# Optimization experiments

Measured on AMD Instinct MI355X. Metric: run time of the kernel, lower is better.

The kernel has to match this reference:

```python
import jax, jax.numpy as jnp
import numpy as np
import math

B, S, D, H = 4, 2048, 768, 12
HD = D // H  # 64


def setup_inputs() -> dict:
    key = jax.random.key(0)
    ks = jax.random.split(key, 9)
    s = 0.02
    return {
        "hidden_states": jax.random.normal(ks[0], (B, S, D), jnp.float32),
        "layout_q": jax.random.normal(ks[1], (B, S, D), jnp.float32),
        "layout_k": jax.random.normal(ks[2], (B, S, D), jnp.float32),
        "attention_mask": jnp.zeros((B, 1, 1, S), jnp.float32),
        "Wq": jax.random.normal(ks[3], (D, D), jnp.float32) * s,
        "bq": jnp.zeros((D,), jnp.float32),
        "Wk": jax.random.normal(ks[4], (D, D), jnp.float32) * s,
        "bk": jnp.zeros((D,), jnp.float32),
        "Wv": jax.random.normal(ks[5], (D, D), jnp.float32) * s,
        "bv": jnp.zeros((D,), jnp.float32),
    }


def _split_heads(x):
    # [B,S,D] -> [B,H,S,HD]
    return x.reshape(B, S, H, HD).transpose(0, 2, 1, 3)


def reference(hidden_states, layout_q, layout_k, attention_mask, Wq, bq, Wk, bk, Wv, bv):
    q = _split_heads(hidden_states @ Wq.T + bq)
    k = _split_heads(hidden_states @ Wk.T + bk)
    v = _split_heads(hidden_states @ Wv.T + bv)
    lq = _split_heads(layout_q)
    lk = _split_heads(layout_k)
    scale = 1.0 / math.sqrt(HD)
    # dual-stream scores: content + layout, both [B,H,S,S]
    scores = (jnp.einsum("bhqd,bhkd->bhqk", q, k)
              + jnp.einsum("bhqd,bhkd->bhqk", lq, lk)) * scale
    scores = scores + attention_mask
    probs = jax.nn.softmax(scores, axis=-1)
    ctx = jnp.einsum("bhqk,bhkd->bhqd", probs, v)
    return ctx.transpose(0, 2, 1, 3).reshape(B, S, D)
```

## Files before the change

kernel.cpp:

```cpp
#include <hip/hip_runtime.h>


typedef __attribute__((ext_vector_type(8))) short short8;
typedef __attribute__((ext_vector_type(4))) short short4v;
typedef __attribute__((ext_vector_type(4))) float floatx4;

#define LOG2E 1.4426950408889634f
#define QSCL 0.18033688011112042f

static constexpr int Sn = 2048, Dn = 768, Hn = 12, BHn = 48;

__device__ __forceinline__ unsigned short f2bf(float f) {
  unsigned u = __float_as_uint(f);
  u += 0x7FFFu + ((u >> 16) & 1u);
  return (unsigned short)(u >> 16);
}

typedef const __attribute__((address_space(1))) unsigned int* gas_t;
typedef __attribute__((address_space(3))) unsigned int* las_t;
__device__ __forceinline__ void async16(const void* g, void* l) {
  __builtin_amdgcn_global_load_lds((gas_t)g, (las_t)l, 16, 0, 0);
}

__device__ __forceinline__ floatx4 mfma16(short4v a, short4v b, floatx4 c) {
#if __has_builtin(__builtin_amdgcn_mfma_f32_16x16x16bf16_1k)
  return __builtin_amdgcn_mfma_f32_16x16x16bf16_1k(a, b, c, 0, 0, 0);
#else
  asm volatile("v_mfma_f32_16x16x16_bf16 %0, %1, %2, %0" : "+v"(c) : "v"(a), "v"(b));
  return c;
#endif
}

__global__ void cast_hs_kernel(const float* __restrict__ in, unsigned short* __restrict__ out, int n4) {
  int i = blockIdx.x * 256 + threadIdx.x;
  if (i >= n4) return;
  float4 v = ((const float4*)in)[i];
  ushort4 o = make_ushort4(f2bf(v.x), f2bf(v.y), f2bf(v.z), f2bf(v.w));
  ((ushort4*)out)[i] = o;
}

__global__ void cast_w_kernel(const float* __restrict__ w0, const float* __restrict__ w1,
                              const float* __restrict__ w2, unsigned short* __restrict__ out) {
  int i = blockIdx.x * 256 + threadIdx.x;
  const float* src = (blockIdx.y == 0) ? w0 : (blockIdx.y == 1) ? w1 : w2;
  float4 v = ((const float4*)src)[i];
  ushort4 o = make_ushort4(f2bf(v.x), f2bf(v.y), f2bf(v.z), f2bf(v.w));
  ((ushort4*)(out + (size_t)blockIdx.y * Dn * Dn))[i] = o;
}

__global__ void pack_layout_kernel(const float* __restrict__ lq, const float* __restrict__ lk,
                                   unsigned short* __restrict__ Qc, unsigned short* __restrict__ Kc) {
  int idx = blockIdx.x * 256 + threadIdx.x;
  const float* src = blockIdx.y ? lk : lq;
  unsigned short* dst = blockIdx.y ? Kc : Qc;
  const float sc = blockIdx.y ? 1.0f : QSCL;
  int d4 = idx & 15;
  int t = idx >> 4;
  int h = t % Hn;
  int bs = t / Hn;
  int b = bs >> 11, s = bs & (Sn - 1);
  float4 v = ((const float4*)src)[idx];
  ushort4 o = make_ushort4(f2bf(v.x * sc), f2bf(v.y * sc), f2bf(v.z * sc), f2bf(v.w * sc));
  size_t off = ((size_t)(b * Hn + h) * Sn + s) * 128 + 64 + d4 * 4;
  *(ushort4*)(dst + off) = o;
}

__global__ __launch_bounds__(256, 2)
void proj_kernel(const unsigned short* __restrict__ X,
                 const unsigned short* __restrict__ Wb,
                 const float* __restrict__ bq, const float* __restrict__ bk, const float* __restrict__ bv,
                 unsigned short* __restrict__ Qc, unsigned short* __restrict__ Kc,
                 unsigned short* __restrict__ Vt) {
  __shared__ __align__(16) unsigned short sMem[16384];
  unsigned short* const sA = sMem;
  unsigned short* const sB = sMem + 8192;

  const int z = blockIdx.z;
  const unsigned short* W = Wb + (size_t)z * Dn * Dn;
  const float* bias = (z == 0) ? bq : (z == 1) ? bk : bv;

  const int t = threadIdx.x;
  const int lane = t & 63, wave = t >> 6;
  const int wm = wave >> 1, wn = wave & 1;
  const int quad = lane >> 4, col15 = lane & 15;
  const int m0 = blockIdx.y * 128, n0 = blockIdx.x * 128;

  const int srow = lane >> 3, schunk = lane & 7;

  floatx4 acc[4][4];
#pragma unroll
  for (int i = 0; i < 4; i++)
#pragma unroll
    for (int j = 0; j < 4; j++) acc[i][j] = (floatx4){0.f, 0.f, 0.f, 0.f};

  for (int k0 = 0; k0 < Dn; k0 += 64) {
    __syncthreads();
#pragma unroll
    for (int c = 0; c < 4; c++) {
      int row = wave * 32 + c * 8 + srow;
      int g = schunk ^ (row & 7);
      async16(X + (size_t)(m0 + row) * Dn + k0 + g * 8, sA + (wave * 32 + c * 8) * 64);
      async16(W + (size_t)(n0 + row) * Dn + k0 + g * 8, sB + (wave * 32 + c * 8) * 64);
    }
    __syncthreads();
#pragma unroll
    for (int kk = 0; kk < 2; kk++) {
      short8 af[4], bf[4];
      const int slot_ = ((kk * 4 + quad) ^ (col15 & 7)) * 8;
#pragma unroll
      for (int i = 0; i < 4; i++)
        af[i] = *(const short8*)(sA + (wm * 64 + i * 16 + col15) * 64 + slot_);
#pragma unroll
      for (int j = 0; j < 4; j++)
        bf[j] = *(const short8*)(sB + (wn * 64 + j * 16 + col15) * 64 + slot_);
#pragma unroll
      for (int i = 0; i < 4; i++)
#pragma unroll
        for (int j = 0; j < 4; j++)
          acc[i][j] = __builtin_amdgcn_mfma_f32_16x16x32_bf16(af[i], bf[j], acc[i][j], 0, 0, 0);
    }
  }

  __syncthreads();
  const int b = m0 >> 11;
  const int s0g = m0 & (Sn - 1);
  const int h0 = n0 >> 6;

  if (z < 2) {
    const float scl = (z == 0) ? QSCL : 1.0f;
    unsigned short* dst0 = (z == 0) ? Qc : Kc;
#pragma unroll
    for (int j = 0; j < 4; j++) {
      int nl = wn * 64 + j * 16 + col15;
      float bias_n = bias[n0 + nl];
#pragma unroll
      for (int i = 0; i < 4; i++) {
        int mb = wm * 64 + i * 16 + quad * 4;
#pragma unroll
        for (int r = 0; r < 4; r++) {
          int m = mb + r;
          sMem[m * 128 + (nl ^ (((m >> 2) & 3) << 4))] = f2bf((acc[i][j][r] + bias_n) * scl);
        }
      }
    }
    __syncthreads();
#pragma unroll
    for (int cc = 0; cc < 8; cc++) {
      int idx = cc * 256 + t;
      int m = idx >> 4, piece = idx & 15;
      int h = h0 + (piece >> 3), d8 = piece & 7;
      short8 v = *(const short8*)(sMem + m * 128 + (piece ^ (((m >> 2) & 3) << 1)) * 8);
      *(short8*)(dst0 + ((size_t)(b * Hn + h) * Sn + s0g + m) * 128 + d8 * 8) = v;
    }
  } else {
#pragma unroll
    for (int j = 0; j < 4; j++) {
      int nl = wn * 64 + j * 16 + col15;
      float bias_n = bias[n0 + nl];
#pragma unroll
      for (int i = 0; i < 4; i++) {
        int mb = wm * 64 + i * 16 + quad * 4;
        ushort4 pk = make_ushort4(f2bf(acc[i][j][0] + bias_n), f2bf(acc[i][j][1] + bias_n),
                                  f2bf(acc[i][j][2] + bias_n), f2bf(acc[i][j][3] + bias_n));
        *(ushort4*)(sMem + nl * 128 + (mb ^ ((nl & 7) << 4))) = pk;
      }
    }
    __syncthreads();
#pragma unroll
    for (int cc = 0; cc < 8; cc++) {
      int idx = cc * 256 + t;
      int nl = idx >> 4, piece = idx & 15;
      int h = h0 + (nl >> 6), d = nl & 63;
      short8 v = *(const short8*)(sMem + nl * 128 + (piece ^ ((nl & 7) << 1)) * 8);
      *(short8*)(Vt + ((size_t)(b * Hn + h) * 64 + d) * Sn + s0g + piece * 8) = v;
    }
  }
}

__global__ __launch_bounds__(256, 3)
void attn_kernel(const unsigned short* __restrict__ Qc,
                 const unsigned short* __restrict__ Kc,
                 const unsigned short* __restrict__ Vt,
                 const float* __restrict__ mask,
                 float* __restrict__ out) {
  __shared__ __align__(16) unsigned short sKc[64 * 128];
  __shared__ __align__(16) unsigned short sVt[64 * 64];
  __shared__ __align__(16) float sMask[Sn];

  const int t = threadIdx.x;
  const int lane = t & 63, wave = t >> 6;
  const int quad = lane >> 4, col15 = lane & 15;

  const int id = blockIdx.x;
  const int slot = id >> 3;
  const int bh = (id & 7) + 8 * (slot >> 4);
  const int q0 = (slot & 15) * 128;
  const int b = bh / Hn, h = bh % Hn;

  const float* mbase = mask + (size_t)b * Sn;
#pragma unroll
  for (int c = 0; c < 2; c++)
    async16(mbase + (c * 256 + wave * 64 + lane) * 4, sMask + (c * 256 + wave * 64) * 4);

  short8 aq[2][4];
  const unsigned short* Qbase = Qc + ((size_t)bh * Sn + q0 + wave * 32) * 128;
#pragma unroll
  for (int jq = 0; jq < 2; jq++)
#pragma unroll
    for (int kk = 0; kk < 4; kk++)
      aq[jq][kk] = *(const short8*)(Qbase + (size_t)(jq * 16 + col15) * 128 + kk * 32 + quad * 8);

  floatx4 OT[4][2];
#pragma unroll
  for (int i = 0; i < 4; i++) {
    OT[i][0] = (floatx4){0.f, 0.f, 0.f, 0.f};
    OT[i][1] = (floatx4){0.f, 0.f, 0.f, 0.f};
  }
  float lsum[2] = {0.f, 0.f};

  const unsigned short* Kbase = Kc + (size_t)bh * Sn * 128;
  const unsigned short* Vbase = Vt + (size_t)bh * 64 * Sn;

  const int krow = lane >> 4, kslot = lane & 15;
  const int vrow = lane >> 3, vslot = lane & 7;

  for (int kt = 0; kt < Sn / 64; kt++) {
    __syncthreads();
#pragma unroll
    for (int c = 0; c < 4; c++) {
      int row = wave * 16 + c * 4 + krow;
      int g = (kslot & 8) | ((kslot ^ row) & 7);
      async16(Kbase + (size_t)(kt * 64 + row) * 128 + g * 8, sKc + (wave * 16 + c * 4) * 128);
    }
#pragma unroll
    for (int c = 0; c < 2; c++) {
      int row = wave * 16 + c * 8 + vrow;
      int g = vslot ^ (row & 7);
      async16(Vbase + (size_t)row * Sn + kt * 64 + g * 8, sVt + (wave * 16 + c * 8) * 64);
    }
    __syncthreads();

    floatx4 sacc[4][2];
#pragma unroll
    for (int jk = 0; jk < 4; jk++) {
      sacc[jk][0] = (floatx4){0.f, 0.f, 0.f, 0.f};
      sacc[jk][1] = (floatx4){0.f, 0.f, 0.f, 0.f};
#pragma unroll
      for (int kk = 0; kk < 4; kk++) {
        int gr = kk * 4 + quad;
        int slot_ = ((gr & 8) | ((gr ^ col15) & 7)) * 8;
        short8 kf = *(const short8*)(sKc + (jk * 16 + col15) * 128 + slot_);
        sacc[jk][0] = __builtin_amdgcn_mfma_f32_16x16x32_bf16(kf, aq[0][kk], sacc[jk][0], 0, 0, 0);
        sacc[jk][1] = __builtin_amdgcn_mfma_f32_16x16x32_bf16(kf, aq[1][kk], sacc[jk][1], 0, 0, 0);
      }
    }

    short4v pvb[2][4];
#pragma unroll
    for (int jk = 0; jk < 4; jk++) {
      float4 mv = *(const float4*)(sMask + kt * 64 + jk * 16 + quad * 4);
      float m0 = mv.x * LOG2E, m1 = mv.y * LOG2E, m2 = mv.z * LOG2E, m3 = mv.w * LOG2E;
#pragma unroll
      for (int jq = 0; jq < 2; jq++) {
        unsigned u0 = __float_as_uint(__builtin_amdgcn_exp2f(sacc[jk][jq][0] + m0)) & 0xFFFF0000u;
        unsigned u1 = __float_as_uint(__builtin_amdgcn_exp2f(sacc[jk][jq][1] + m1)) & 0xFFFF0000u;
        unsigned u2 = __float_as_uint(__builtin_amdgcn_exp2f(sacc[jk][jq][2] + m2)) & 0xFFFF0000u;
        unsigned u3 = __float_as_uint(__builtin_amdgcn_exp2f(sacc[jk][jq][3] + m3)) & 0xFFFF0000u;
        lsum[jq] += (__uint_as_float(u0) + __uint_as_float(u1)) +
                    (__uint_as_float(u2) + __uint_as_float(u3));
        int2 pk;
        pk.x = (int)((u0 >> 16) | u1);
        pk.y = (int)((u2 >> 16) | u3);
        pvb[jq][jk] = *(short4v*)&pk;
      }
    }

#pragma unroll
    for (int i = 0; i < 4; i++) {
      int row = i * 16 + col15;
#pragma unroll
      for (int jk = 0; jk < 4; jk++) {
        int gi = (jk * 2 + (quad >> 1)) ^ (row & 7);
        short4v vf = *(const short4v*)(sVt + row * 64 + gi * 8 + (quad & 1) * 4);
        OT[i][0] = mfma16(vf, pvb[0][jk], OT[i][0]);
        OT[i][1] = mfma16(vf, pvb[1][jk], OT[i][1]);
      }
    }
  }

  float linv[2];
#pragma unroll
  for (int jq = 0; jq < 2; jq++) {
    float s_ = lsum[jq];
    s_ += __shfl_xor(s_, 16);
    s_ += __shfl_xor(s_, 32);
    linv[jq] = 1.0f / s_;
  }
#pragma unroll
  for (int jq = 0; jq < 2; jq++) {
    float* obase = out + ((size_t)b * Sn + q0 + wave * 32 + jq * 16 + col15) * Dn + h * 64 + quad * 4;
#pragma unroll
    for (int i = 0; i < 4; i++) {
      float4 o;
      o.x = OT[i][jq][0] * linv[jq];
      o.y = OT[i][jq][1] * linv[jq];
      o.z = OT[i][jq][2] * linv[jq];
      o.w = OT[i][jq][3] * linv[jq];
      *(float4*)(obase + i * 16) = o;
    }
  }
}

extern "C" void kernel_launch(void* const* d_in, const int* in_sizes, int n_in,
                              void* d_out, int out_size, void* d_ws, size_t ws_size,
                              hipStream_t stream) {
  const float* hs   = (const float*)d_in[0];
  const float* lq   = (const float*)d_in[1];
  const float* lk   = (const float*)d_in[2];
  const float* mask = (const float*)d_in[3];
  const float* Wq   = (const float*)d_in[4];
  const float* bq   = (const float*)d_in[5];
  const float* Wk   = (const float*)d_in[6];
  const float* bk   = (const float*)d_in[7];
  const float* Wv   = (const float*)d_in[8];
  const float* bv   = (const float*)d_in[9];
  float* out = (float*)d_out;

  char* ws = (char*)d_ws;
  unsigned short* Xbf = (unsigned short*)ws;
  unsigned short* Wbf = (unsigned short*)(ws + 12582912);
  unsigned short* Qc  = (unsigned short*)(ws + 12582912 + 3538944);
  unsigned short* Kc  = Qc + (size_t)BHn * Sn * 128;
  unsigned short* Vt  = Kc + (size_t)BHn * Sn * 128;

  cast_hs_kernel<<<6144, 256, 0, stream>>>(hs, Xbf, 1572864);
  cast_w_kernel<<<dim3(576, 3), 256, 0, stream>>>(Wq, Wk, Wv, Wbf);
  pack_layout_kernel<<<dim3(6144, 2), 256, 0, stream>>>(lq, lk, Qc, Kc);
  proj_kernel<<<dim3(6, 64, 3), 256, 0, stream>>>(Xbf, Wbf, bq, bk, bv, Qc, Kc, Vt);
  attn_kernel<<<768, 256, 0, stream>>>(Qc, Kc, Vt, mask, out);
}
```

Baseline: 272.9 us.

## Fuse fp32 casts and layout packing into projection; use 16x16x32 MFMA for PV

Drops the three standalone cast and pack kernels. The projection GEMM now loads fp32 X and W directly, converts them to bf16 in registers before storing to LDS, and packs the scaled layout_q/layout_k halves into Qc/Kc in its epilogue. In attention, probabilities are staged through a padded LDS buffer so the PV product can use the wider 16x16x32 bf16 MFMA instead of 16x16x16. This removes kernel launches and intermediate bf16 round trips through memory. In exchange, the GEMM loses its async global-to-LDS loads in favour of synchronous register loads with no prefetch, and attention uses more LDS per block, which may reduce occupancy.

After: 281.8 us. 3.3% more time.

```diff
diff --git a/kernel.cpp b/kernel.cpp
--- a/kernel.cpp
+++ b/kernel.cpp
@@ -1,8 +1,8 @@
 #include <hip/hip_runtime.h>
+#include <hip/hip_bf16.h>
 
 
 typedef __attribute__((ext_vector_type(8))) short short8;
-typedef __attribute__((ext_vector_type(4))) short short4v;
 typedef __attribute__((ext_vector_type(4))) float floatx4;
 
 #define LOG2E 1.4426950408889634f
@@ -16,59 +16,31 @@
   return (unsigned short)(u >> 16);
 }
 
+__device__ __forceinline__ short8 cvt8(float4 a, float4 b) {
+  union { __hip_bfloat162 h; int i; } u0, u1, u2, u3;
+  u0.h = __float22bfloat162_rn(float2{a.x, a.y});
+  u1.h = __float22bfloat162_rn(float2{a.z, a.w});
+  u2.h = __float22bfloat162_rn(float2{b.x, b.y});
+  u3.h = __float22bfloat162_rn(float2{b.z, b.w});
+  short8 r;
+  ((int*)&r)[0] = u0.i; ((int*)&r)[1] = u1.i;
+  ((int*)&r)[2] = u2.i; ((int*)&r)[3] = u3.i;
+  return r;
+}
+
 typedef const __attribute__((address_space(1))) unsigned int* gas_t;
 typedef __attribute__((address_space(3))) unsigned int* las_t;
 __device__ __forceinline__ void async16(const void* g, void* l) {
   __builtin_amdgcn_global_load_lds((gas_t)g, (las_t)l, 16, 0, 0);
 }
 
-__device__ __forceinline__ floatx4 mfma16(short4v a, short4v b, floatx4 c) {
-#if __has_builtin(__builtin_amdgcn_mfma_f32_16x16x16bf16_1k)
-  return __builtin_amdgcn_mfma_f32_16x16x16bf16_1k(a, b, c, 0, 0, 0);
-#else
-  asm volatile("v_mfma_f32_16x16x16_bf16 %0, %1, %2, %0" : "+v"(c) : "v"(a), "v"(b));
-  return c;
-#endif
-}
-
-__global__ void cast_hs_kernel(const float* __restrict__ in, unsigned short* __restrict__ out, int n4) {
-  int i = blockIdx.x * 256 + threadIdx.x;
-  if (i >= n4) return;
-  float4 v = ((const float4*)in)[i];
-  ushort4 o = make_ushort4(f2bf(v.x), f2bf(v.y), f2bf(v.z), f2bf(v.w));
-  ((ushort4*)out)[i] = o;
-}
-
-__global__ void cast_w_kernel(const float* __restrict__ w0, const float* __restrict__ w1,
-                              const float* __restrict__ w2, unsigned short* __restrict__ out) {
-  int i = blockIdx.x * 256 + threadIdx.x;
-  const float* src = (blockIdx.y == 0) ? w0 : (blockIdx.y == 1) ? w1 : w2;
-  float4 v = ((const float4*)src)[i];
-  ushort4 o = make_ushort4(f2bf(v.x), f2bf(v.y), f2bf(v.z), f2bf(v.w));
-  ((ushort4*)(out + (size_t)blockIdx.y * Dn * Dn))[i] = o;
-}
-
-__global__ void pack_layout_kernel(const float* __restrict__ lq, const float* __restrict__ lk,
-                                   unsigned short* __restrict__ Qc, unsigned short* __restrict__ Kc) {
-  int idx = blockIdx.x * 256 + threadIdx.x;
-  const float* src = blockIdx.y ? lk : lq;
-  unsigned short* dst = blockIdx.y ? Kc : Qc;
-  const float sc = blockIdx.y ? 1.0f : QSCL;
-  int d4 = idx & 15;
-  int t = idx >> 4;
-  int h = t % Hn;
-  int bs = t / Hn;
-  int b = bs >> 11, s = bs & (Sn - 1);
-  float4 v = ((const float4*)src)[idx];
-  ushort4 o = make_ushort4(f2bf(v.x * sc), f2bf(v.y * sc), f2bf(v.z * sc), f2bf(v.w * sc));
-  size_t off = ((size_t)(b * Hn + h) * Sn + s) * 128 + 64 + d4 * 4;
-  *(ushort4*)(dst + off) = o;
-}
-
 __global__ __launch_bounds__(256, 2)
-void proj_kernel(const unsigned short* __restrict__ X,
-                 const unsigned short* __restrict__ Wb,
-                 const float* __restrict__ bq, const float* __restrict__ bk, const float* __restrict__ bv,
+void proj_kernel(const float* __restrict__ X,
+                 const float* __restrict__ Wq, const float* __restrict__ Wk,
+                 const float* __restrict__ Wv,
+                 const float* __restrict__ bq, const float* __restrict__ bk,
+                 const float* __restrict__ bv,
+                 const float* __restrict__ LQ, const float* __restrict__ LK,
                  unsigned short* __restrict__ Qc, unsigned short* __restrict__ Kc,
                  unsigned short* __restrict__ Vt) {
   __shared__ __align__(16) unsigned short sMem[16384];
@@ -76,7 +48,7 @@
   unsigned short* const sB = sMem + 8192;
 
   const int z = blockIdx.z;
-  const unsigned short* W = Wb + (size_t)z * Dn * Dn;
+  const float* W = (z == 0) ? Wq : (z == 1) ? Wk : Wv;
   const float* bias = (z == 0) ? bq : (z == 1) ? bk : bv;
 
   const int t = threadIdx.x;
@@ -85,8 +57,6 @@
   const int quad = lane >> 4, col15 = lane & 15;
   const int m0 = blockIdx.y * 128, n0 = blockIdx.x * 128;
 
-  const int srow = lane >> 3, schunk = lane & 7;
-
   floatx4 acc[4][4];
 #pragma unroll
   for (int i = 0; i < 4; i++)
@@ -94,13 +64,24 @@
     for (int j = 0; j < 4; j++) acc[i][j] = (floatx4){0.f, 0.f, 0.f, 0.f};
 
   for (int k0 = 0; k0 < Dn; k0 += 64) {
-    __syncthreads();
+    float4 xa[4][2], xb[4][2];
 #pragma unroll
     for (int c = 0; c < 4; c++) {
-      int row = wave * 32 + c * 8 + srow;
-      int g = schunk ^ (row & 7);
-      async16(X + (size_t)(m0 + row) * Dn + k0 + g * 8, sA + (wave * 32 + c * 8) * 64);
-      async16(W + (size_t)(n0 + row) * Dn + k0 + g * 8, sB + (wave * 32 + c * 8) * 64);
+      int idx = c * 256 + t;
+      int row = idx >> 3, sl = idx & 7;
+      int gd = sl ^ (row & 7);
+      const float* pa = X + (size_t)(m0 + row) * Dn + k0 + gd * 8;
+      const float* pb = W + (size_t)(n0 + row) * Dn + k0 + gd * 8;
+      xa[c][0] = *(const float4*)pa; xa[c][1] = *(const float4*)(pa + 4);
+      xb[c][0] = *(const float4*)pb; xb[c][1] = *(const float4*)(pb + 4);
+    }
+    __syncthreads();
+#pragma unroll
+    for (int c = 0; c < 4; c++) {
+      int idx = c * 256 + t;
+      int row = idx >> 3, sl = idx & 7;
+      *(short8*)(sA + row * 64 + sl * 8) = cvt8(xa[c][0], xa[c][1]);
+      *(short8*)(sB + row * 64 + sl * 8) = cvt8(xb[c][0], xb[c][1]);
     }
     __syncthreads();
 #pragma unroll
@@ -144,6 +125,7 @@
       }
     }
     __syncthreads();
+    const float* lsrc = (z == 0) ? LQ : LK;
 #pragma unroll
     for (int cc = 0; cc < 8; cc++) {
       int idx = cc * 256 + t;
@@ -152,6 +134,17 @@
       short8 v = *(const short8*)(sMem + m * 128 + (piece ^ (((m >> 2) & 3) << 1)) * 8);
       *(short8*)(dst0 + ((size_t)(b * Hn + h) * Sn + s0g + m) * 128 + d8 * 8) = v;
     }
+#pragma unroll
+    for (int cc = 0; cc < 8; cc++) {
+      int idx = cc * 256 + t;
+      int m = idx >> 4, piece = idx & 15;
+      int h = h0 + (piece >> 3), d8 = piece & 7;
+      const float* p = lsrc + ((size_t)b * Sn + s0g + m) * Dn + n0 + piece * 8;
+      float4 v0 = *(const float4*)p, v1 = *(const float4*)(p + 4);
+      v0.x *= scl; v0.y *= scl; v0.z *= scl; v0.w *= scl;
+      v1.x *= scl; v1.y *= scl; v1.z *= scl; v1.w *= scl;
+      *(short8*)(dst0 + ((size_t)(b * Hn + h) * Sn + s0g + m) * 128 + 64 + d8 * 8) = cvt8(v0, v1);
+    }
   } else {
 #pragma unroll
     for (int j = 0; j < 4; j++) {
@@ -183,9 +176,11 @@
                  const unsigned short* __restrict__ Vt,
                  const float* __restrict__ mask,
                  float* __restrict__ out) {
+  constexpr int LDP = 72;
   __shared__ __align__(16) unsigned short sKc[64 * 128];
   __shared__ __align__(16) unsigned short sVt[64 * 64];
   __shared__ __align__(16) float sMask[Sn];
+  __shared__ __align__(16) unsigned short sP[128 * LDP];
 
   const int t = threadIdx.x;
   const int lane = t & 63, wave = t >> 6;
@@ -255,35 +250,35 @@
       }
     }
 
-    short4v pvb[2][4];
 #pragma unroll
     for (int jk = 0; jk < 4; jk++) {
       float4 mv = *(const float4*)(sMask + kt * 64 + jk * 16 + quad * 4);
-      float m0 = mv.x * LOG2E, m1 = mv.y * LOG2E, m2 = mv.z * LOG2E, m3 = mv.w * LOG2E;
+      float m0v = mv.x * LOG2E, m1v = mv.y * LOG2E, m2v = mv.z * LOG2E, m3v = mv.w * LOG2E;
 #pragma unroll
       for (int jq = 0; jq < 2; jq++) {
-        unsigned u0 = __float_as_uint(__builtin_amdgcn_exp2f(sacc[jk][jq][0] + m0)) & 0xFFFF0000u;
-        unsigned u1 = __float_as_uint(__builtin_amdgcn_exp2f(sacc[jk][jq][1] + m1)) & 0xFFFF0000u;
-        unsigned u2 = __float_as_uint(__builtin_amdgcn_exp2f(sacc[jk][jq][2] + m2)) & 0xFFFF0000u;
-        unsigned u3 = __float_as_uint(__builtin_amdgcn_exp2f(sacc[jk][jq][3] + m3)) & 0xFFFF0000u;
+        unsigned u0 = __float_as_uint(__builtin_amdgcn_exp2f(sacc[jk][jq][0] + m0v)) & 0xFFFF0000u;
+        unsigned u1 = __float_as_uint(__builtin_amdgcn_exp2f(sacc[jk][jq][1] + m1v)) & 0xFFFF0000u;
+        unsigned u2 = __float_as_uint(__builtin_amdgcn_exp2f(sacc[jk][jq][2] + m2v)) & 0xFFFF0000u;
+        unsigned u3 = __float_as_uint(__builtin_amdgcn_exp2f(sacc[jk][jq][3] + m3v)) & 0xFFFF0000u;
         lsum[jq] += (__uint_as_float(u0) + __uint_as_float(u1)) +
                     (__uint_as_float(u2) + __uint_as_float(u3));
         int2 pk;
         pk.x = (int)((u0 >> 16) | u1);
         pk.y = (int)((u2 >> 16) | u3);
-        pvb[jq][jk] = *(short4v*)&pk;
-      }
-    }
-
-#pragma unroll
-    for (int i = 0; i < 4; i++) {
-      int row = i * 16 + col15;
-#pragma unroll
-      for (int jk = 0; jk < 4; jk++) {
-        int gi = (jk * 2 + (quad >> 1)) ^ (row & 7);
-        short4v vf = *(const short4v*)(sVt + row * 64 + gi * 8 + (quad & 1) * 4);
-        OT[i][0] = mfma16(vf, pvb[0][jk], OT[i][0]);
-        OT[i][1] = mfma16(vf, pvb[1][jk], OT[i][1]);
+        *(int2*)(sP + (wave * 32 + jq * 16 + col15) * LDP + jk * 16 + quad * 4) = pk;
+      }
+    }
+
+#pragma unroll
+    for (int jk2 = 0; jk2 < 2; jk2++) {
+      short8 pf0 = *(const short8*)(sP + (wave * 32 + col15) * LDP + jk2 * 32 + quad * 8);
+      short8 pf1 = *(const short8*)(sP + (wave * 32 + 16 + col15) * LDP + jk2 * 32 + quad * 8);
+#pragma unroll
+      for (int i = 0; i < 4; i++) {
+        int row = i * 16 + col15;
+        short8 vf = *(const short8*)(sVt + row * 64 + ((jk2 * 4 + quad) ^ (row & 7)) * 8);
+        OT[i][0] = __builtin_amdgcn_mfma_f32_16x16x32_bf16(vf, pf0, OT[i][0], 0, 0, 0);
+        OT[i][1] = __builtin_amdgcn_mfma_f32_16x16x32_bf16(vf, pf1, OT[i][1], 0, 0, 0);
       }
     }
   }
@@ -327,15 +322,10 @@
   float* out = (float*)d_out;
 
   char* ws = (char*)d_ws;
-  unsigned short* Xbf = (unsigned short*)ws;
-  unsigned short* Wbf = (unsigned short*)(ws + 12582912);
-  unsigned short* Qc  = (unsigned short*)(ws + 12582912 + 3538944);
-  unsigned short* Kc  = Qc + (size_t)BHn * Sn * 128;
-  unsigned short* Vt  = Kc + (size_t)BHn * Sn * 128;
-
-  cast_hs_kernel<<<6144, 256, 0, stream>>>(hs, Xbf, 1572864);
-  cast_w_kernel<<<dim3(576, 3), 256, 0, stream>>>(Wq, Wk, Wv, Wbf);
-  pack_layout_kernel<<<dim3(6144, 2), 256, 0, stream>>>(lq, lk, Qc, Kc);
-  proj_kernel<<<dim3(6, 64, 3), 256, 0, stream>>>(Xbf, Wbf, bq, bk, bv, Qc, Kc, Vt);
+  unsigned short* Qc = (unsigned short*)ws;
+  unsigned short* Kc = Qc + (size_t)BHn * Sn * 128;
+  unsigned short* Vt = Kc + (size_t)BHn * Sn * 128;
+
+  proj_kernel<<<dim3(6, 64, 3), 256, 0, stream>>>(hs, Wq, Wk, Wv, bq, bk, bv, lq, lk, Qc, Kc, Vt);
   attn_kernel<<<768, 256, 0, stream>>>(Qc, Kc, Vt, mask, out);
 }
```
